# Performance work log

Hardware: AMD Instinct MI355X
Metric: run time of the kernel (lower is better)

The kernel has to match this reference:

```python
import jax, jax.numpy as jnp
import numpy as np

RESIDUAL_WEIGHT = 0.3
TEMPERATURE = 0.07
EPS = 1e-12


def setup_inputs() -> dict:
    key = jax.random.key(0)
    features = jax.random.normal(key, (4, 64, 64, 384), dtype=jnp.float32)
    return {"features": features}


def reference(features):
    B, H, W, D = features.shape
    x = features.reshape(B, H * W, D)                      # (B, N, D)
    # F.normalize(dim=-1): x / max(||x||, eps)
    norm = jnp.linalg.norm(x, axis=-1, keepdims=True)
    xn = x / jnp.maximum(norm, EPS)
    # cosine-similarity correlation matrix, scaled by temperature
    corr = jnp.einsum("bnd,bmd->bnm", xn, xn) / TEMPERATURE  # (B, N, N)
    attn = jax.nn.softmax(corr, axis=-1)
    attended = jnp.einsum("bnm,bmd->bnd", attn, x)         # (B, N, D)
    out = x + RESIDUAL_WEIGHT * attended
    return out.reshape(B, H, W, D)
```

## Files before the change

kernel.cpp:

```cpp
#include <hip/hip_runtime.h>
#include <hip/hip_bf16.h>
#include <stdint.h>

typedef __bf16 bf16_t;
typedef __bf16 bf16x8 __attribute__((ext_vector_type(8)));
typedef float f32x4 __attribute__((ext_vector_type(4)));

#define BB 4
#define NN 4096
#define DD 384
#define KBLK 32
#define NKT (NN / KBLK)
#define NROWS (BB * NN)
#define SCALEC 20.609929155556627f

__global__ __launch_bounds__(256) void norm_kernel(const float* __restrict__ x,
                                                   bf16_t* __restrict__ xn) {
    int row  = blockIdx.x * 4 + (threadIdx.x >> 6);
    int lane = threadIdx.x & 63;
    const float* xr = x + (size_t)row * DD;
    float v[6];
    float ss = 0.f;
#pragma unroll
    for (int j = 0; j < 6; ++j) { v[j] = xr[lane + j * 64]; ss += v[j] * v[j]; }
#pragma unroll
    for (int m = 1; m < 64; m <<= 1) ss += __shfl_xor(ss, m);
    float inv = 1.0f / fmaxf(sqrtf(ss), 1e-12f);
    bf16_t* o = xn + (size_t)row * DD;
#pragma unroll
    for (int j = 0; j < 6; ++j) o[lane + j * 64] = (bf16_t)(v[j] * inv);
}

__global__ __launch_bounds__(256) void transpose_kernel(const float* __restrict__ x,
                                                        bf16_t* __restrict__ xvT) {
    int bid = blockIdx.x;
    int dt = bid % (DD / 64);
    int nt = (bid / (DD / 64)) % (NN / 64);
    int b  = bid / ((DD / 64) * (NN / 64));
    __shared__ float tile[64][65];
    int t = threadIdx.x;
    const float* src = x + ((size_t)b * NN + (size_t)nt * 64) * DD + dt * 64;
#pragma unroll
    for (int j = 0; j < 4; ++j) {
        int lin = j * 256 + t;
        int nl = lin >> 4;
        int dc = (lin & 15) * 4;
        const float4 f = *(const float4*)(src + (size_t)nl * DD + dc);
        tile[nl][dc + 0] = f.x; tile[nl][dc + 1] = f.y;
        tile[nl][dc + 2] = f.z; tile[nl][dc + 3] = f.w;
    }
    __syncthreads();
    bf16_t* dst = xvT + ((size_t)b * DD + (size_t)dt * 64) * NN + (size_t)nt * 64;
#pragma unroll
    for (int j = 0; j < 2; ++j) {
        int lin = j * 256 + t;
        int dl = lin >> 3;
        int nc = (lin & 7) * 8;
        bf16x8 v;
#pragma unroll
        for (int jj = 0; jj < 8; ++jj) v[jj] = (bf16_t)tile[nc + jj][dl];
        *(bf16x8*)(dst + (size_t)dl * NN + nc) = v;
    }
}

__device__ __forceinline__ void load_lds16(const void* g, void* l) {
    __builtin_amdgcn_global_load_lds((const __attribute__((address_space(1))) uint32_t*)g,
                                     (__attribute__((address_space(3))) uint32_t*)l,
                                     16, 0, 0);
}

template <int S, bool DIRECT>
__global__ __launch_bounds__(256, 2) void attn_kernel(const float* __restrict__ x,
                                                      const bf16_t* __restrict__ xn,
                                                      const bf16_t* __restrict__ xvT,
                                                      float* __restrict__ out,
                                                      float* __restrict__ Opart,
                                                      float* __restrict__ lpart) {
    constexpr int TPS = NKT / S;
    __shared__ __align__(16) char Ks[2][24576];
    __shared__ __align__(16) char VL[24576];
    __shared__ __align__(16) bf16_t Pb[4 * 16 * KBLK];

    const int tid = threadIdx.x;
    const int w = tid >> 6, l = tid & 63;
    const int lo = l & 15, g = l >> 4;

    const int bid = blockIdx.x;
    const int s_idx = (S == 2) ? (bid & 1) : 0;
    const int qbid  = (S == 2) ? (bid >> 1) : bid;
    const int b  = (qbid >> 1) & 3;
    const int qt = (qbid >> 3) | ((qbid & 1) << 5);
    const int kt0 = s_idx * TPS;

    const size_t qrow = (size_t)b * NN + (size_t)qt * 64 + w * 16 + lo;
    const bf16_t* qp = xn + qrow * DD + g * 8;
    bf16x8 qf[12];
#pragma unroll
    for (int c = 0; c < 12; ++c) qf[c] = *(const bf16x8*)(qp + c * 32);

    const f32x4 fzero = {0.f, 0.f, 0.f, 0.f};
    f32x4 O[24];
#pragma unroll
    for (int i = 0; i < 24; ++i) O[i] = fzero;
    float lacc[4] = {0.f, 0.f, 0.f, 0.f};

    const char* xnb  = (const char*)xn;
    const char* xvTb = (const char*)xvT;
    char* Ksb = (char*)Ks;
    char* VLb = (char*)VL;
    bf16_t* Pw = Pb + w * 16 * KBLK;

    {
        const size_t kgbase = ((size_t)b * NN + (size_t)kt0 * KBLK) * (DD * 2);
#pragma unroll
        for (int i = 0; i < 6; ++i) {
            int ci = i * 256 + tid;
            int key = ci & 31, cg = ci >> 5;
            const char* gp = xnb + kgbase + key * (DD * 2) + cg * 16;
            load_lds16(gp, (void*)(Ksb + (i * 256 + (w << 6)) * 16));
        }
    }
    __syncthreads();

    for (int t = 0; t < TPS; ++t) {
        const int p = t & 1;
        const int kt = kt0 + t;
        {
            const size_t vgbase = (size_t)b * ((size_t)DD * NN * 2) + (size_t)kt * (KBLK * 2);
#pragma unroll
            for (int i = 0; i < 6; ++i) {
                int ci = i * 256 + tid;
                int lo4 = ci & 15, g4 = (ci >> 4) & 3, dt = ci >> 6;
                const char* gp = xvTb + vgbase + (size_t)(dt * 16 + lo4) * (NN * 2) + g4 * 16;
                load_lds16(gp, (void*)(VLb + (i * 256 + (w << 6)) * 16));
            }
        }
        __builtin_amdgcn_sched_barrier(0);
        {
            const size_t kgbase = ((size_t)b * NN + (size_t)(kt + 1) * KBLK) * (DD * 2);
            char* Kdst = Ksb + (p ^ 1) * 24576;
#pragma unroll
            for (int i = 0; i < 6; ++i) {
                int ci = i * 256 + tid;
                int key = ci & 31, cg = ci >> 5;
                const char* gp = xnb + kgbase + key * (DD * 2) + cg * 16;
                load_lds16(gp, (void*)(Kdst + (i * 256 + (w << 6)) * 16));
            }
        }
        __builtin_amdgcn_sched_barrier(0);

        const char* kb = Ksb + p * 24576 + (g << 9) + (lo << 4);
        f32x4 s0 = fzero, s1 = fzero;
#pragma unroll
        for (int c = 0; c < 12; ++c) {
            bf16x8 kf0 = *(const bf16x8*)(kb + c * 2048);
            bf16x8 kf1 = *(const bf16x8*)(kb + c * 2048 + 256);
            s0 = __builtin_amdgcn_mfma_f32_16x16x32_bf16(qf[c], kf0, s0, 0, 0, 0);
            s1 = __builtin_amdgcn_mfma_f32_16x16x32_bf16(qf[c], kf1, s1, 0, 0, 0);
        }

        float p0[4], p1[4];
#pragma unroll
        for (int r = 0; r < 4; ++r) {
            p0[r] = exp2f(fmaf(s0[r], SCALEC, -SCALEC));
            p1[r] = exp2f(fmaf(s1[r], SCALEC, -SCALEC));
            lacc[r] += p0[r] + p1[r];
        }

#pragma unroll
        for (int r = 0; r < 4; ++r) {
            Pw[(g * 4 + r) * KBLK + lo]      = (bf16_t)p0[r];
            Pw[(g * 4 + r) * KBLK + lo + 16] = (bf16_t)p1[r];
        }
        bf16x8 pa = *(const bf16x8*)(Pw + lo * KBLK + g * 8);

        asm volatile("s_waitcnt vmcnt(6)" ::: "memory");
        __builtin_amdgcn_sched_barrier(0);
        __builtin_amdgcn_s_barrier();
        __builtin_amdgcn_sched_barrier(0);

        const char* vbL = VLb + (g << 8) + (lo << 4);
#pragma unroll
        for (int dt = 0; dt < 24; ++dt) {
            bf16x8 vf = *(const bf16x8*)(vbL + dt * 1024);
            O[dt] = __builtin_amdgcn_mfma_f32_16x16x32_bf16(pa, vf, O[dt], 0, 0, 0);
        }
        __syncthreads();
    }

#pragma unroll
    for (int mk = 1; mk < 16; mk <<= 1) {
#pragma unroll
        for (int r = 0; r < 4; ++r) lacc[r] += __shfl_xor(lacc[r], mk);
    }
    const int grow0 = b * NN + qt * 64 + w * 16;
    if (DIRECT) {
        float inv[4];
#pragma unroll
        for (int r = 0; r < 4; ++r) inv[r] = 0.3f / lacc[r];
#pragma unroll
        for (int dt = 0; dt < 24; ++dt) {
#pragma unroll
            for (int r = 0; r < 4; ++r) {
                size_t idx = (size_t)(grow0 + g * 4 + r) * DD + dt * 16 + lo;
                out[idx] = x[idx] + O[dt][r] * inv[r];
            }
        }
    } else {
        float* Ob = Opart + (size_t)s_idx * NROWS * DD;
#pragma unroll
        for (int dt = 0; dt < 24; ++dt) {
#pragma unroll
            for (int r = 0; r < 4; ++r) {
                Ob[(size_t)(grow0 + g * 4 + r) * DD + dt * 16 + lo] = O[dt][r];
            }
        }
        if (lo == 0) {
#pragma unroll
            for (int r = 0; r < 4; ++r)
                lpart[(size_t)s_idx * NROWS + grow0 + g * 4 + r] = lacc[r];
        }
    }
}

__global__ __launch_bounds__(256) void merge_kernel(const float* __restrict__ x,
                                                    const float* __restrict__ Opart,
                                                    const float* __restrict__ lpart,
                                                    float* __restrict__ out) {
    int row  = blockIdx.x * 4 + (threadIdx.x >> 6);
    int lane = threadIdx.x & 63;
    float lsum = lpart[row] + lpart[NROWS + row];
    float inv = 0.3f / lsum;
    size_t base = (size_t)row * DD;
    const float* O0 = Opart + base;
    const float* O1 = Opart + (size_t)NROWS * DD + base;
#pragma unroll
    for (int j = 0; j < 6; ++j) {
        int d = lane + j * 64;
        out[base + d] = x[base + d] + (O0[d] + O1[d]) * inv;
    }
}

extern "C" void kernel_launch(void* const* d_in, const int* in_sizes, int n_in,
                              void* d_out, int out_size, void* d_ws, size_t ws_size,
                              hipStream_t stream) {
    const float* x = (const float*)d_in[0];
    float* out = (float*)d_out;
    char* ws = (char*)d_ws;

    const size_t xn_bytes = (size_t)BB * NN * DD * 2;
    bf16_t* xn  = (bf16_t*)ws;
    bf16_t* xvT = (bf16_t*)(ws + xn_bytes);
    float* Opart = (float*)(ws + 2 * xn_bytes);
    const size_t Opart_bytes = (size_t)2 * NROWS * DD * 4;
    float* lpart = (float*)(ws + 2 * xn_bytes + Opart_bytes);
    const size_t need2 = 2 * xn_bytes + Opart_bytes + (size_t)2 * NROWS * 4;

    norm_kernel<<<(BB * NN) / 4, 256, 0, stream>>>(x, xn);
    transpose_kernel<<<BB * (NN / 64) * (DD / 64), 256, 0, stream>>>(x, xvT);
    if (ws_size >= need2) {
        attn_kernel<2, false><<<512, 256, 0, stream>>>(x, xn, xvT, out, Opart, lpart);
        merge_kernel<<<NROWS / 4, 256, 0, stream>>>(x, Opart, lpart, out);
    } else {
        attn_kernel<1, true><<<256, 256, 0, stream>>>(x, xn, xvT, out, nullptr, nullptr);
    }
}
```

Measured before the change: 277.7 us.

## Restructure attention kernel to 32x32 MFMA with 64-key tiles and shared P

The attention kernel now uses 64-key tiles and 32x32x16 bf16 MFMAs. Waves are split into query-group by key-half for QK^T, and each wave owns a 96-column slice of D for PV. V fragments are loaded straight from global memory into registers instead of staged through LDS, and probabilities are written to a swizzled shared P tile that all waves read. Row sums are now computed from the bf16 P tile. The aim is fewer MFMA issues per FLOP and more operand reuse, at the cost of extra barriers per tile, single-buffered K staging, and register pressure from 24 Q fragments plus 12 V fragments.

Result: slower. 808.0 us (+190.9%).

```diff
diff --git a/kernel.cpp b/kernel.cpp
--- a/kernel.cpp
+++ b/kernel.cpp
@@ -5,12 +5,13 @@
 typedef __bf16 bf16_t;
 typedef __bf16 bf16x8 __attribute__((ext_vector_type(8)));
 typedef float f32x4 __attribute__((ext_vector_type(4)));
+typedef float f32x16 __attribute__((ext_vector_type(16)));
 
 #define BB 4
 #define NN 4096
 #define DD 384
-#define KBLK 32
-#define NKT (NN / KBLK)
+#define KBLK 64
+#define NT (NN / KBLK)
 #define NROWS (BB * NN)
 #define SCALEC 20.609929155556627f
 
@@ -69,156 +70,180 @@
                                      16, 0, 0);
 }
 
-template <int S, bool DIRECT>
+template <bool SPLIT>
 __global__ __launch_bounds__(256, 2) void attn_kernel(const float* __restrict__ x,
                                                       const bf16_t* __restrict__ xn,
                                                       const bf16_t* __restrict__ xvT,
                                                       float* __restrict__ out,
                                                       float* __restrict__ Opart,
                                                       float* __restrict__ lpart) {
-    constexpr int TPS = NKT / S;
-    __shared__ __align__(16) char Ks[2][24576];
-    __shared__ __align__(16) char VL[24576];
-    __shared__ __align__(16) bf16_t Pb[4 * 16 * KBLK];
+    constexpr int TPS = SPLIT ? (NT / 2) : NT;
+    __shared__ __align__(16) char Ks[49152];
+    __shared__ __align__(16) char Pb[16384];
 
     const int tid = threadIdx.x;
     const int w = tid >> 6, l = tid & 63;
-    const int lo = l & 15, g = l >> 4;
+    const int l31 = l & 31, hi = l >> 5;
+    const int qg = w >> 1, kh = w & 1;
 
     const int bid = blockIdx.x;
-    const int s_idx = (S == 2) ? (bid & 1) : 0;
-    const int qbid  = (S == 2) ? (bid >> 1) : bid;
-    const int b  = (qbid >> 1) & 3;
-    const int qt = (qbid >> 3) | ((qbid & 1) << 5);
+    int b, qi, s_idx;
+    if (SPLIT) {
+        b = (bid & 7) >> 1; s_idx = bid & 1; qi = bid >> 3;
+    } else {
+        b = (bid >> 1) & 3; s_idx = 0; qi = (bid >> 3) | ((bid & 1) << 5);
+    }
     const int kt0 = s_idx * TPS;
-
-    const size_t qrow = (size_t)b * NN + (size_t)qt * 64 + w * 16 + lo;
-    const bf16_t* qp = xn + qrow * DD + g * 8;
-    bf16x8 qf[12];
-#pragma unroll
-    for (int c = 0; c < 12; ++c) qf[c] = *(const bf16x8*)(qp + c * 32);
-
-    const f32x4 fzero = {0.f, 0.f, 0.f, 0.f};
-    f32x4 O[24];
-#pragma unroll
-    for (int i = 0; i < 24; ++i) O[i] = fzero;
-    float lacc[4] = {0.f, 0.f, 0.f, 0.f};
+    const int qrow0 = b * NN + qi * 64;
 
     const char* xnb  = (const char*)xn;
     const char* xvTb = (const char*)xvT;
     char* Ksb = (char*)Ks;
-    char* VLb = (char*)VL;
-    bf16_t* Pw = Pb + w * 16 * KBLK;
-
-    {
-        const size_t kgbase = ((size_t)b * NN + (size_t)kt0 * KBLK) * (DD * 2);
-#pragma unroll
-        for (int i = 0; i < 6; ++i) {
-            int ci = i * 256 + tid;
-            int key = ci & 31, cg = ci >> 5;
-            const char* gp = xnb + kgbase + key * (DD * 2) + cg * 16;
-            load_lds16(gp, (void*)(Ksb + (i * 256 + (w << 6)) * 16));
-        }
-    }
-    __syncthreads();
+    char* Pbb = (char*)Pb;
+
+    const bf16_t* qp = xn + (size_t)(qrow0 + qg * 32 + l31) * DD + hi * 8;
+    bf16x8 qf[24];
+#pragma unroll
+    for (int c = 0; c < 24; ++c) qf[c] = *(const bf16x8*)(qp + c * 16);
+
+    f32x16 O0, O1, O2, O3, O4, O5;
+    O0 = 0.f; O1 = 0.f; O2 = 0.f; O3 = 0.f; O4 = 0.f; O5 = 0.f;
+    float lacc = 0.f;
+
+#define STAGE_K(KT) { \
+    const size_t kg = ((size_t)b * NN + (size_t)(KT) * KBLK) * (DD * 2); \
+    _Pragma("unroll") \
+    for (int i = 0; i < 12; ++i) { \
+        int idx = i * 256 + tid; int key = idx & 63; int c2h = idx >> 6; \
+        load_lds16(xnb + kg + (size_t)key * (DD * 2) + c2h * 16, \
+                   (void*)(Ksb + (size_t)(i * 256 + (w << 6)) * 16)); \
+    } }
+
+    STAGE_K(kt0);
+
+    const char* kB = Ksb + (size_t)(hi * 64 + kh * 32 + l31) * 16;
+    const int psw = (l31 & 15) << 4;
+    const int rsrow = tid >> 2, rsseg = tid & 3;
+    const int rswz = (rsrow & 15) << 4;
+    const int kcol2 = (kh * 32 + l31) * 2;
 
     for (int t = 0; t < TPS; ++t) {
-        const int p = t & 1;
         const int kt = kt0 + t;
+        asm volatile("s_waitcnt vmcnt(0)" ::: "memory");
+        __builtin_amdgcn_sched_barrier(0);
+        __builtin_amdgcn_s_barrier();
+        __builtin_amdgcn_sched_barrier(0);
+
+        bf16x8 vf[3][4];
         {
-            const size_t vgbase = (size_t)b * ((size_t)DD * NN * 2) + (size_t)kt * (KBLK * 2);
-#pragma unroll
-            for (int i = 0; i < 6; ++i) {
-                int ci = i * 256 + tid;
-                int lo4 = ci & 15, g4 = (ci >> 4) & 3, dt = ci >> 6;
-                const char* gp = xvTb + vgbase + (size_t)(dt * 16 + lo4) * (NN * 2) + g4 * 16;
-                load_lds16(gp, (void*)(VLb + (i * 256 + (w << 6)) * 16));
+            const char* vB = xvTb + (((size_t)(b * DD + w * 96 + l31) * NN)
+                                     + (size_t)kt * KBLK + hi * 8) * 2;
+#pragma unroll
+            for (int dt = 0; dt < 3; ++dt)
+#pragma unroll
+                for (int kc = 0; kc < 4; ++kc)
+                    vf[dt][kc] = *(const bf16x8*)(vB + (size_t)dt * 32 * (NN * 2) + kc * 32);
+        }
+
+        f32x16 s = 0.f;
+#pragma unroll
+        for (int c = 0; c < 24; ++c) {
+            bf16x8 kf = *(const bf16x8*)(kB + c * 2048);
+            s = __builtin_amdgcn_mfma_f32_32x32x16_bf16(qf[c], kf, s, 0, 0, 0);
+        }
+
+        __builtin_amdgcn_sched_barrier(0);
+        __builtin_amdgcn_s_barrier();
+        __builtin_amdgcn_sched_barrier(0);
+
+        {
+            int ktn = kt + 1; if (ktn > NT - 1) ktn = NT - 1;
+            STAGE_K(ktn);
+        }
+        __builtin_amdgcn_sched_barrier(0);
+
+#pragma unroll
+        for (int r = 0; r < 16; ++r) {
+            float p = exp2f(fmaf(s[r], SCALEC, -SCALEC));
+            int q = qg * 32 + 4 * hi + (r & 3) + 8 * (r >> 2);
+            int off = q * 256 + (kcol2 ^ ((q & 15) << 4));
+            *(bf16_t*)(Pbb + off) = (bf16_t)p;
+        }
+        asm volatile("s_waitcnt lgkmcnt(0)" ::: "memory");
+        __builtin_amdgcn_sched_barrier(0);
+        __builtin_amdgcn_s_barrier();
+        __builtin_amdgcn_sched_barrier(0);
+
+        {
+            const char* rb = Pbb + rsrow * 256;
+            bf16x8 a = *(const bf16x8*)(rb + ((rsseg * 32) ^ rswz));
+            bf16x8 c = *(const bf16x8*)(rb + ((rsseg * 32 + 16) ^ rswz));
+            float ps = 0.f;
+#pragma unroll
+            for (int e = 0; e < 8; ++e) ps += (float)a[e] + (float)c[e];
+            lacc += ps;
+        }
+
+#pragma unroll
+        for (int g2 = 0; g2 < 2; ++g2) {
+            const char* paB = Pbb + (g2 * 32 + l31) * 256;
+#pragma unroll
+            for (int kc = 0; kc < 4; ++kc) {
+                bf16x8 pa = *(const bf16x8*)(paB + ((kc * 32 + hi * 16) ^ psw));
+                if (g2 == 0) {
+                    O0 = __builtin_amdgcn_mfma_f32_32x32x16_bf16(pa, vf[0][kc], O0, 0, 0, 0);
+                    O1 = __builtin_amdgcn_mfma_f32_32x32x16_bf16(pa, vf[1][kc], O1, 0, 0, 0);
+                    O2 = __builtin_amdgcn_mfma_f32_32x32x16_bf16(pa, vf[2][kc], O2, 0, 0, 0);
+                } else {
+                    O3 = __builtin_amdgcn_mfma_f32_32x32x16_bf16(pa, vf[0][kc], O3, 0, 0, 0);
+                    O4 = __builtin_amdgcn_mfma_f32_32x32x16_bf16(pa, vf[1][kc], O4, 0, 0, 0);
+                    O5 = __builtin_amdgcn_mfma_f32_32x32x16_bf16(pa, vf[2][kc], O5, 0, 0, 0);
+                }
             }
         }
-        __builtin_amdgcn_sched_barrier(0);
-        {
-            const size_t kgbase = ((size_t)b * NN + (size_t)(kt + 1) * KBLK) * (DD * 2);
-            char* Kdst = Ksb + (p ^ 1) * 24576;
-#pragma unroll
-            for (int i = 0; i < 6; ++i) {
-                int ci = i * 256 + tid;
-                int key = ci & 31, cg = ci >> 5;
-                const char* gp = xnb + kgbase + key * (DD * 2) + cg * 16;
-                load_lds16(gp, (void*)(Kdst + (i * 256 + (w << 6)) * 16));
+    }
+#undef STAGE_K
+
+    lacc += __shfl_xor(lacc, 1);
+    lacc += __shfl_xor(lacc, 2);
+
+    if (SPLIT) {
+        if ((tid & 3) == 0) lpart[(size_t)s_idx * NROWS + qrow0 + rsrow] = lacc;
+        float* Ob = Opart + (size_t)s_idx * NROWS * DD;
+        const f32x16* Os[6] = {&O0, &O1, &O2, &O3, &O4, &O5};
+#pragma unroll
+        for (int g2 = 0; g2 < 2; ++g2) {
+#pragma unroll
+            for (int dt = 0; dt < 3; ++dt) {
+                const f32x16& Ot = *Os[g2 * 3 + dt];
+                int dcol = w * 96 + dt * 32 + l31;
+#pragma unroll
+                for (int r = 0; r < 16; ++r) {
+                    int q = g2 * 32 + 4 * hi + (r & 3) + 8 * (r >> 2);
+                    Ob[(size_t)(qrow0 + q) * DD + dcol] = Ot[r];
+                }
             }
         }
-        __builtin_amdgcn_sched_barrier(0);
-
-        const char* kb = Ksb + p * 24576 + (g << 9) + (lo << 4);
-        f32x4 s0 = fzero, s1 = fzero;
-#pragma unroll
-        for (int c = 0; c < 12; ++c) {
-            bf16x8 kf0 = *(const bf16x8*)(kb + c * 2048);
-            bf16x8 kf1 = *(const bf16x8*)(kb + c * 2048 + 256);
-            s0 = __builtin_amdgcn_mfma_f32_16x16x32_bf16(qf[c], kf0, s0, 0, 0, 0);
-            s1 = __builtin_amdgcn_mfma_f32_16x16x32_bf16(qf[c], kf1, s1, 0, 0, 0);
-        }
-
-        float p0[4], p1[4];
-#pragma unroll
-        for (int r = 0; r < 4; ++r) {
-            p0[r] = exp2f(fmaf(s0[r], SCALEC, -SCALEC));
-            p1[r] = exp2f(fmaf(s1[r], SCALEC, -SCALEC));
-            lacc[r] += p0[r] + p1[r];
-        }
-
-#pragma unroll
-        for (int r = 0; r < 4; ++r) {
-            Pw[(g * 4 + r) * KBLK + lo]      = (bf16_t)p0[r];
-            Pw[(g * 4 + r) * KBLK + lo + 16] = (bf16_t)p1[r];
-        }
-        bf16x8 pa = *(const bf16x8*)(Pw + lo * KBLK + g * 8);
-
-        asm volatile("s_waitcnt vmcnt(6)" ::: "memory");
-        __builtin_amdgcn_sched_barrier(0);
-        __builtin_amdgcn_s_barrier();
-        __builtin_amdgcn_sched_barrier(0);
-
-        const char* vbL = VLb + (g << 8) + (lo << 4);
-#pragma unroll
-        for (int dt = 0; dt < 24; ++dt) {
-            bf16x8 vf = *(const bf16x8*)(vbL + dt * 1024);
-            O[dt] = __builtin_amdgcn_mfma_f32_16x16x32_bf16(pa, vf, O[dt], 0, 0, 0);
-        }
-        __syncthreads();
-    }
-
-#pragma unroll
-    for (int mk = 1; mk < 16; mk <<= 1) {
-#pragma unroll
-        for (int r = 0; r < 4; ++r) lacc[r] += __shfl_xor(lacc[r], mk);
-    }
-    const int grow0 = b * NN + qt * 64 + w * 16;
-    if (DIRECT) {
-        float inv[4];
-#pragma unroll
-        for (int r = 0; r < 4; ++r) inv[r] = 0.3f / lacc[r];
-#pragma unroll
-        for (int dt = 0; dt < 24; ++dt) {
-#pragma unroll
-            for (int r = 0; r < 4; ++r) {
-                size_t idx = (size_t)(grow0 + g * 4 + r) * DD + dt * 16 + lo;
-                out[idx] = x[idx] + O[dt][r] * inv[r];
+    } else {
+        __builtin_amdgcn_s_barrier();
+        float* lb = (float*)Pbb;
+        if ((tid & 3) == 0) lb[rsrow] = lacc;
+        asm volatile("s_waitcnt lgkmcnt(0)" ::: "memory");
+        __builtin_amdgcn_s_barrier();
+        const f32x16* Os[6] = {&O0, &O1, &O2, &O3, &O4, &O5};
+#pragma unroll
+        for (int g2 = 0; g2 < 2; ++g2) {
+#pragma unroll
+            for (int dt = 0; dt < 3; ++dt) {
+                const f32x16& Ot = *Os[g2 * 3 + dt];
+                int dcol = w * 96 + dt * 32 + l31;
+#pragma unroll
+                for (int r = 0; r < 16; ++r) {
+                    int q = g2 * 32 + 4 * hi + (r & 3) + 8 * (r >> 2);
+                    size_t idx = (size_t)(qrow0 + q) * DD + dcol;
+                    out[idx] = x[idx] + Ot[r] * (0.3f / lb[q]);
+                }
             }
-        }
-    } else {
-        float* Ob = Opart + (size_t)s_idx * NROWS * DD;
-#pragma unroll
-        for (int dt = 0; dt < 24; ++dt) {
-#pragma unroll
-            for (int r = 0; r < 4; ++r) {
-                Ob[(size_t)(grow0 + g * 4 + r) * DD + dt * 16 + lo] = O[dt][r];
-            }
-        }
-        if (lo == 0) {
-#pragma unroll
-            for (int r = 0; r < 4; ++r)
-                lpart[(size_t)s_idx * NROWS + grow0 + g * 4 + r] = lacc[r];
         }
     }
 }
@@ -259,9 +284,9 @@
     norm_kernel<<<(BB * NN) / 4, 256, 0, stream>>>(x, xn);
     transpose_kernel<<<BB * (NN / 64) * (DD / 64), 256, 0, stream>>>(x, xvT);
     if (ws_size >= need2) {
-        attn_kernel<2, false><<<512, 256, 0, stream>>>(x, xn, xvT, out, Opart, lpart);
+        attn_kernel<true><<<512, 256, 0, stream>>>(x, xn, xvT, out, Opart, lpart);
         merge_kernel<<<NROWS / 4, 256, 0, stream>>>(x, Opart, lpart, out);
     } else {
-        attn_kernel<1, true><<<256, 256, 0, stream>>>(x, xn, xvT, out, nullptr, nullptr);
-    }
-}
+        attn_kernel<false><<<256, 256, 0, stream>>>(x, xn, xvT, out, nullptr, nullptr);
+    }
+}
```

## Overlap first K tile load with Q fetch and tighten barrier waits in attention loop

Applied to the files above, without the earlier changes.

Moves the Q fragment register loads ahead of the initial K staging and drops the prologue __syncthreads, so the first K tile load overlaps with setup. Inside the loop it waits on vmcnt(12) plus a bare s_barrier instead of a full syncthreads, clamps the prefetch index so the last iteration loads a valid tile, and reads the P fragment after the barrier with lgkmcnt(0). It also swaps exp2f for the hardware exp2 builtin. These aim to cut pipeline stalls and barrier overhead, at the cost of a redundant final K load and tighter reliance on correct wait counts.

After: 279.9 us. No clear change (+0.8%).

```diff
diff --git a/kernel.cpp b/kernel.cpp
--- a/kernel.cpp
+++ b/kernel.cpp
@@ -86,23 +86,18 @@
     const int lo = l & 15, g = l >> 4;
 
     const int bid = blockIdx.x;
-    const int s_idx = (S == 2) ? (bid & 1) : 0;
-    const int qbid  = (S == 2) ? (bid >> 1) : bid;
-    const int b  = (qbid >> 1) & 3;
-    const int qt = (qbid >> 3) | ((qbid & 1) << 5);
+    int b, qt, s_idx;
+    if (S == 2) {
+        s_idx = bid & 1;
+        int qbid = bid >> 1;
+        b  = (qbid >> 1) & 3;
+        qt = (qbid >> 3) | ((qbid & 1) << 5);
+    } else {
+        s_idx = 0;
+        b  = (bid >> 1) & 3;
+        qt = (bid >> 3) | ((bid & 1) << 5);
+    }
     const int kt0 = s_idx * TPS;
-
-    const size_t qrow = (size_t)b * NN + (size_t)qt * 64 + w * 16 + lo;
-    const bf16_t* qp = xn + qrow * DD + g * 8;
-    bf16x8 qf[12];
-#pragma unroll
-    for (int c = 0; c < 12; ++c) qf[c] = *(const bf16x8*)(qp + c * 32);
-
-    const f32x4 fzero = {0.f, 0.f, 0.f, 0.f};
-    f32x4 O[24];
-#pragma unroll
-    for (int i = 0; i < 24; ++i) O[i] = fzero;
-    float lacc[4] = {0.f, 0.f, 0.f, 0.f};
 
     const char* xnb  = (const char*)xn;
     const char* xvTb = (const char*)xvT;
@@ -110,46 +105,59 @@
     char* VLb = (char*)VL;
     bf16_t* Pw = Pb + w * 16 * KBLK;
 
-    {
-        const size_t kgbase = ((size_t)b * NN + (size_t)kt0 * KBLK) * (DD * 2);
-#pragma unroll
-        for (int i = 0; i < 6; ++i) {
-            int ci = i * 256 + tid;
-            int key = ci & 31, cg = ci >> 5;
-            const char* gp = xnb + kgbase + key * (DD * 2) + cg * 16;
-            load_lds16(gp, (void*)(Ksb + (i * 256 + (w << 6)) * 16));
-        }
-    }
-    __syncthreads();
+    const size_t qrow = (size_t)b * NN + (size_t)qt * 64 + w * 16 + lo;
+    const bf16_t* qp = xn + qrow * DD + g * 8;
+    bf16x8 qf[12];
+#pragma unroll
+    for (int c = 0; c < 12; ++c) qf[c] = *(const bf16x8*)(qp + c * 32);
+
+    const f32x4 fzero = {0.f, 0.f, 0.f, 0.f};
+    f32x4 O[24];
+#pragma unroll
+    for (int i = 0; i < 24; ++i) O[i] = fzero;
+    float lacc[4] = {0.f, 0.f, 0.f, 0.f};
+
+#define STAGE_K(KT, BUF) { \
+    const size_t kg = ((size_t)b * NN + (size_t)(KT) * KBLK) * (DD * 2); \
+    char* kdst = Ksb + (BUF) * 24576; \
+    _Pragma("unroll") \
+    for (int i = 0; i < 6; ++i) { \
+        int ci = i * 256 + tid; int key = ci & 31; int cg = ci >> 5; \
+        load_lds16(xnb + kg + (size_t)key * (DD * 2) + cg * 16, \
+                   (void*)(kdst + (size_t)(i * 256 + (w << 6)) * 16)); \
+    } }
+
+#define STAGE_V(KT) { \
+    const size_t vg = (size_t)b * ((size_t)DD * NN * 2) + (size_t)(KT) * (KBLK * 2); \
+    _Pragma("unroll") \
+    for (int i = 0; i < 6; ++i) { \
+        int ci = i * 256 + tid; int lo4 = ci & 15; int g4v = (ci >> 4) & 3; int dtv = ci >> 6; \
+        load_lds16(xvTb + vg + (size_t)(dtv * 16 + lo4) * (NN * 2) + g4v * 16, \
+                   (void*)(VLb + (size_t)(i * 256 + (w << 6)) * 16)); \
+    } }
+
+    STAGE_K(kt0, 0);
+
+    const char* kB  = Ksb + (g << 9) + (lo << 4);
+    const char* vbL = VLb + (g << 8) + (lo << 4);
+    const bf16_t* pap = Pw + lo * KBLK + g * 8;
 
     for (int t = 0; t < TPS; ++t) {
+        const int kt = kt0 + t;
         const int p = t & 1;
-        const int kt = kt0 + t;
-        {
-            const size_t vgbase = (size_t)b * ((size_t)DD * NN * 2) + (size_t)kt * (KBLK * 2);
-#pragma unroll
-            for (int i = 0; i < 6; ++i) {
-                int ci = i * 256 + tid;
-                int lo4 = ci & 15, g4 = (ci >> 4) & 3, dt = ci >> 6;
-                const char* gp = xvTb + vgbase + (size_t)(dt * 16 + lo4) * (NN * 2) + g4 * 16;
-                load_lds16(gp, (void*)(VLb + (i * 256 + (w << 6)) * 16));
-            }
-        }
-        __builtin_amdgcn_sched_barrier(0);
-        {
-            const size_t kgbase = ((size_t)b * NN + (size_t)(kt + 1) * KBLK) * (DD * 2);
-            char* Kdst = Ksb + (p ^ 1) * 24576;
-#pragma unroll
-            for (int i = 0; i < 6; ++i) {
-                int ci = i * 256 + tid;
-                int key = ci & 31, cg = ci >> 5;
-                const char* gp = xnb + kgbase + key * (DD * 2) + cg * 16;
-                load_lds16(gp, (void*)(Kdst + (i * 256 + (w << 6)) * 16));
-            }
-        }
-        __builtin_amdgcn_sched_barrier(0);
-
-        const char* kb = Ksb + p * 24576 + (g << 9) + (lo << 4);
+
+        STAGE_V(kt);
+        __builtin_amdgcn_sched_barrier(0);
+        int ktn = kt + 1; if (ktn > NKT - 1) ktn = NKT - 1;
+        STAGE_K(ktn, p ^ 1);
+        __builtin_amdgcn_sched_barrier(0);
+
+        asm volatile("s_waitcnt vmcnt(12)" ::: "memory");
+        __builtin_amdgcn_sched_barrier(0);
+        __builtin_amdgcn_s_barrier();
+        __builtin_amdgcn_sched_barrier(0);
+
+        const char* kb = kB + p * 24576;
         f32x4 s0 = fzero, s1 = fzero;
 #pragma unroll
         for (int c = 0; c < 12; ++c) {
@@ -162,38 +170,42 @@
         float p0[4], p1[4];
 #pragma unroll
         for (int r = 0; r < 4; ++r) {
-            p0[r] = exp2f(fmaf(s0[r], SCALEC, -SCALEC));
-            p1[r] = exp2f(fmaf(s1[r], SCALEC, -SCALEC));
+            p0[r] = __builtin_amdgcn_exp2f(fmaf(s0[r], SCALEC, -SCALEC));
+            p1[r] = __builtin_amdgcn_exp2f(fmaf(s1[r], SCALEC, -SCALEC));
             lacc[r] += p0[r] + p1[r];
         }
-
 #pragma unroll
         for (int r = 0; r < 4; ++r) {
             Pw[(g * 4 + r) * KBLK + lo]      = (bf16_t)p0[r];
             Pw[(g * 4 + r) * KBLK + lo + 16] = (bf16_t)p1[r];
         }
-        bf16x8 pa = *(const bf16x8*)(Pw + lo * KBLK + g * 8);
-
-        asm volatile("s_waitcnt vmcnt(6)" ::: "memory");
+
+        asm volatile("s_waitcnt vmcnt(6) lgkmcnt(0)" ::: "memory");
         __builtin_amdgcn_sched_barrier(0);
         __builtin_amdgcn_s_barrier();
         __builtin_amdgcn_sched_barrier(0);
 
-        const char* vbL = VLb + (g << 8) + (lo << 4);
+        bf16x8 pa = *(const bf16x8*)pap;
+
 #pragma unroll
         for (int dt = 0; dt < 24; ++dt) {
             bf16x8 vf = *(const bf16x8*)(vbL + dt * 1024);
             O[dt] = __builtin_amdgcn_mfma_f32_16x16x32_bf16(pa, vf, O[dt], 0, 0, 0);
         }
-        __syncthreads();
-    }
+
+        __builtin_amdgcn_sched_barrier(0);
+        __builtin_amdgcn_s_barrier();
+        __builtin_amdgcn_sched_barrier(0);
+    }
+#undef STAGE_K
+#undef STAGE_V
 
 #pragma unroll
     for (int mk = 1; mk < 16; mk <<= 1) {
 #pragma unroll
         for (int r = 0; r < 4; ++r) lacc[r] += __shfl_xor(lacc[r], mk);
     }
-    const int grow0 = b * NN + qt * 64 + w * 16;
+    const int orow0 = b * NN + qt * 64 + w * 16;
     if (DIRECT) {
         float inv[4];
 #pragma unroll
@@ -202,23 +214,23 @@
         for (int dt = 0; dt < 24; ++dt) {
 #pragma unroll
             for (int r = 0; r < 4; ++r) {
-                size_t idx = (size_t)(grow0 + g * 4 + r) * DD + dt * 16 + lo;
+                size_t idx = (size_t)(orow0 + g * 4 + r) * DD + dt * 16 + lo;
                 out[idx] = x[idx] + O[dt][r] * inv[r];
             }
         }
     } else {
+        if (lo == 0) {
+#pragma unroll
+            for (int r = 0; r < 4; ++r)
+                lpart[(size_t)s_idx * NROWS + orow0 + g * 4 + r] = lacc[r];
+        }
         float* Ob = Opart + (size_t)s_idx * NROWS * DD;
 #pragma unroll
         for (int dt = 0; dt < 24; ++dt) {
 #pragma unroll
             for (int r = 0; r < 4; ++r) {
-                Ob[(size_t)(grow0 + g * 4 + r) * DD + dt * 16 + lo] = O[dt][r];
+                Ob[(size_t)(orow0 + g * 4 + r) * DD + dt * 16 + lo] = O[dt][r];
             }
-        }
-        if (lo == 0) {
-#pragma unroll
-            for (int r = 0; r < 4; ++r)
-                lpart[(size_t)s_idx * NROWS + grow0 + g * 4 + r] = lacc[r];
         }
     }
 }
```
